# Optimization experiments

Measured on AMD Instinct MI355X. Metric: run time of the kernel, lower is better.

The kernel has to match this reference:

```python
import jax, jax.numpy as jnp
import numpy as np

K_TOP = 16
TEMP = 1.0
EPS = 1e-9

def setup_inputs() -> dict:
    key = jax.random.key(0)
    k1, k2, k3 = jax.random.split(key, 3)
    B, H, N, D = 4, 8, 2048, 64
    q = jax.random.normal(k1, (B, H, N, D), dtype=jnp.float32)
    k = jax.random.normal(k2, (B, H, N, D), dtype=jnp.float32)
    u = jax.random.uniform(k3, (B, N, N), dtype=jnp.float32)
    return {"q": q, "k": k, "u": u}

def reference(q, k, u):
    # q, k: [B, H, N, D]; u: uniform noise [B, N, N]
    d_head = q.shape[-1]
    scale = 1.0 / jnp.sqrt(jnp.asarray(d_head, dtype=q.dtype))
    # [B, H, N, N] scores, then mean over heads -> [B, N, N]
    attn_scores = jnp.einsum('bhnd,bhmd->bhnm', q, k) * scale
    logits = attn_scores.mean(axis=1)
    gumbel = -jnp.log(-jnp.log(u + EPS) + EPS)
    probs = jax.nn.softmax((logits + gumbel) / TEMP, axis=-1)
    topk_vals = jax.lax.top_k(probs, K_TOP)[0]          # [B, N, K]
    thresh = topk_vals.min(axis=-1, keepdims=True)      # [B, N, 1]
    sparse_mask = (probs >= thresh).astype(probs.dtype)
    return sparse_mask[:, None, :, :]                   # [B, 1, N, N]
```

## Files before the change

### kernel.cpp

```cpp
#include <hip/hip_runtime.h>
#include <math.h>

#define BB 4
#define HH 8
#define NN 2048
#define DD 64
#define KTOP 16
#define CUT_MARGIN 1e-3f

typedef _Float16 half_t;
typedef __attribute__((ext_vector_type(8))) _Float16 half8;
typedef __attribute__((ext_vector_type(4))) float floatx4;

__global__ __launch_bounds__(256, 2) void gemm_conv(const float* __restrict__ q,
                                                    const float* __restrict__ kk,
                                                    float* __restrict__ L) {
    const int flat = blockIdx.x;
    const int swz  = (flat & 7) * 128 + (flat >> 3);
    const int j0 = (swz & 15) * 128;
    const int i0 = ((swz >> 4) & 15) * 128;
    const int b  = swz >> 8;

    const int tid  = threadIdx.x;
    const int wave = __builtin_amdgcn_readfirstlane(tid >> 6);
    const int lane = tid & 63;
    const int wr = wave >> 1, wc = wave & 1;
    const int lm = lane & 15, quad = lane >> 4;

    __shared__ __align__(16) half_t Ah[8192];
    __shared__ __align__(16) half_t Al[8192];
    __shared__ __align__(16) half_t Bh[8192];
    __shared__ __align__(16) half_t Bl[8192];

    const float* gA = q  + ((size_t)(b * HH) * NN + i0) * DD;
    const float* gB = kk + ((size_t)(b * HH) * NN + j0) * DD;

    floatx4 acc1[4][4], acc2[4][4];
#pragma unroll
    for (int tr = 0; tr < 4; ++tr)
#pragma unroll
        for (int tc = 0; tc < 4; ++tc) {
            acc1[tr][tc] = (floatx4)0.0f;
            acc2[tr][tc] = (floatx4)0.0f;
        }

    for (int hh = 0; hh < HH; ++hh) {
        const float* ga = gA + (size_t)hh * (NN * DD);
        const float* gb = gB + (size_t)hh * (NN * DD);

        __syncthreads();

        float4 v0[8], v1[8];
#pragma unroll
        for (int i = 0; i < 4; ++i) {
            const int p = i * 256 + tid;
            v0[i]     = *(const float4*)(ga + (size_t)p * 8);
            v1[i]     = *(const float4*)(ga + (size_t)p * 8 + 4);
            v0[4 + i] = *(const float4*)(gb + (size_t)p * 8);
            v1[4 + i] = *(const float4*)(gb + (size_t)p * 8 + 4);
        }
#pragma unroll
        for (int i = 0; i < 8; ++i) {
            const int p  = (i & 3) * 256 + tid;
            const int r  = p >> 3;
            const int u8 = p & 7;
            const int off = (u8 >> 2) * 4096 + (r >> 3) * 256 +
                            (u8 & 3) * 64 + (r & 7) * 8;
            half_t* dh = (i < 4) ? Ah : Bh;
            half_t* dl = (i < 4) ? Al : Bl;
            float a[8] = {v0[i].x, v0[i].y, v0[i].z, v0[i].w,
                          v1[i].x, v1[i].y, v1[i].z, v1[i].w};
            half8 h, l;
#pragma unroll
            for (int e = 0; e < 8; ++e) {
                half_t hv = (half_t)a[e];
                h[e] = hv;
                l[e] = (half_t)((a[e] - (float)hv) * 2048.0f);
            }
            *(half8*)&dh[off] = h;
            *(half8*)&dl[off] = l;
        }

        __syncthreads();

#pragma unroll
        for (int ks = 0; ks < 2; ++ks) {
            half8 fah[4], fal[4], fbh[4], fbl[4];
#pragma unroll
            for (int t = 0; t < 4; ++t) {
                const int am = wr * 64 + t * 16 + lm;
                const int bm = wc * 64 + t * 16 + lm;
                const int ai = ks * 4096 + ((am >> 3) << 8) + (quad << 6) + ((am & 7) << 3);
                const int bi = ks * 4096 + ((bm >> 3) << 8) + (quad << 6) + ((bm & 7) << 3);
                fah[t] = *(const half8*)&Ah[ai];
                fal[t] = *(const half8*)&Al[ai];
                fbh[t] = *(const half8*)&Bh[bi];
                fbl[t] = *(const half8*)&Bl[bi];
            }
            __builtin_amdgcn_s_setprio(1);
#pragma unroll
            for (int tr = 0; tr < 4; ++tr)
#pragma unroll
                for (int tc = 0; tc < 4; ++tc) {
                    acc1[tr][tc] = __builtin_amdgcn_mfma_f32_16x16x32_f16(
                        fah[tr], fbh[tc], acc1[tr][tc], 0, 0, 0);
                    acc2[tr][tc] = __builtin_amdgcn_mfma_f32_16x16x32_f16(
                        fah[tr], fbl[tc], acc2[tr][tc], 0, 0, 0);
                    acc2[tr][tc] = __builtin_amdgcn_mfma_f32_16x16x32_f16(
                        fal[tr], fbh[tc], acc2[tr][tc], 0, 0, 0);
                }
            __builtin_amdgcn_s_setprio(0);
        }
    }

    const float s1 = 0.015625f;
    const float s2 = 0.015625f / 2048.0f;
#pragma unroll
    for (int tr = 0; tr < 4; ++tr)
#pragma unroll
        for (int r = 0; r < 4; ++r) {
            const int grow = i0 + wr * 64 + tr * 16 + quad * 4 + r;
            float* Lp = L + ((size_t)b * NN + grow) * NN + j0 + wc * 64 + lm;
#pragma unroll
            for (int tc = 0; tc < 4; ++tc)
                Lp[tc * 16] = acc1[tr][tc][r] * s1 + acc2[tr][tc][r] * s2;
        }
}

__device__ __forceinline__ unsigned long long flip64(double x) {
    unsigned long long v = (unsigned long long)__double_as_longlong(x);
    return v ^ ((0ULL - (v >> 63)) | 0x8000000000000000ULL);
}
__device__ __forceinline__ double unflip64(unsigned long long k) {
    unsigned long long v = (k >> 63) ? (k ^ 0x8000000000000000ULL) : ~k;
    return __longlong_as_double((long long)v);
}

__global__ __launch_bounds__(256) void topk_mask(float* __restrict__ LM,
                                                 const float* __restrict__ u) {
    const int wave = threadIdx.x >> 6;
    const int lane = threadIdx.x & 63;
    const int row  = blockIdx.x * 4 + wave;
    float* lrow = LM + (size_t)row * NN;
    const float* urow = u + (size_t)row * NN;

    __shared__ int s_idx[4][64];

    float z[32];
    unsigned hard = 0;
    float4 lb = *(const float4*)(lrow + lane * 4);
    float4 ub = *(const float4*)(urow + lane * 4);
#pragma unroll
    for (int e = 0; e < 8; ++e) {
        float4 lnx, unx;
        if (e < 7) {
            lnx = *(const float4*)(lrow + (e + 1) * 256 + lane * 4);
            unx = *(const float4*)(urow + (e + 1) * 256 + lane * 4);
        }
        const float* ls = (const float*)&lb;
        const float* us = (const float*)&ub;
#pragma unroll
        for (int s = 0; s < 4; ++s) {
            float w = -__logf(us[s] + 1e-9f);
            z[e * 4 + s] = ls[s] - __logf(w + 1e-9f);
            hard |= (us[s] > 0.999f ? 1u : 0u) << (e * 4 + s);
        }
        lb = lnx; ub = unx;
    }

    float v = z[0];
#pragma unroll
    for (int r = 1; r < 32; ++r) v = fmaxf(v, z[r]);
#pragma unroll
    for (int kS = 2; kS <= 64; kS <<= 1) {
#pragma unroll
        for (int j = kS >> 1; j > 0; j >>= 1) {
            float o = __shfl_xor(v, j, 64);
            bool asc = ((lane & kS) == 0);
            bool lower = ((lane & j) == 0);
            float mn = fminf(v, o), mx = fmaxf(v, o);
            v = (asc == lower) ? mn : mx;
        }
    }
    const float cut = __shfl(v, 48, 64) - CUT_MARGIN;

    int c = 0;
#pragma unroll
    for (int r = 0; r < 32; ++r) {
        bool p = (z[r] >= cut);
        unsigned long long m = __ballot(p);
        if (p) {
            int slot = c + __popcll(m & ((1ULL << lane) - 1ULL));
            if (slot < 64) s_idx[wave][slot] = (r >> 2) * 256 + lane * 4 + (r & 3);
        }
        c += __popcll(m);
    }
    if (c > 64) c = 64;

    unsigned long long key = 0xFFFFFFFFFFFFFFFFULL;
    if (lane < c) {
        int idx = s_idx[wave][lane];
        double uu = (double)urow[idx] + 1e-9;
        double w  = -log(uu);
        double g  = -log(w + 1e-9);
        key = flip64((double)lrow[idx] + g);
    }
#pragma unroll
    for (int kS = 2; kS <= 64; kS <<= 1) {
#pragma unroll
        for (int j = kS >> 1; j > 0; j >>= 1) {
            unsigned long long o = __shfl_xor(key, j, 64);
            bool asc = ((lane & kS) == 0);
            bool lower = ((lane & j) == 0);
            unsigned long long mn = (key < o) ? key : o;
            unsigned long long mx = (key < o) ? o : key;
            key = (asc == lower) ? mn : mx;
        }
    }
    const double thresh = unflip64(__shfl(key, c - KTOP, 64));

    const float t_hi = (float)thresh + 3e-4f;
    const float t_lo = (float)thresh - 3e-4f;
    unsigned bm = hard;
#pragma unroll
    for (int r = 0; r < 32; ++r)
        bm |= ((z[r] <= t_hi && z[r] >= t_lo) ? 1u : 0u) << r;
    while (bm) {
        int t = __builtin_ctz(bm);
        bm &= bm - 1;
        const int idx = (t >> 2) * 256 + lane * 4 + (t & 3);
        double uu = (double)urow[idx] + 1e-9;
        double w  = -log(uu);
        double g  = -log(w + 1e-9);
        double z64 = (double)lrow[idx] + g;
        z[t] = (z64 >= thresh) ? 1.0e30f : -1.0e30f;
    }

#pragma unroll
    for (int e = 0; e < 8; ++e) {
        float o[4];
#pragma unroll
        for (int s = 0; s < 4; ++s)
            o[s] = (z[e * 4 + s] > t_hi) ? 1.0f : 0.0f;
        *(float4*)(lrow + e * 256 + lane * 4) = *(float4*)o;
    }
}

extern "C" void kernel_launch(void* const* d_in, const int* in_sizes, int n_in,
                              void* d_out, int out_size, void* d_ws, size_t ws_size,
                              hipStream_t stream) {
    const float* q = (const float*)d_in[0];
    const float* k = (const float*)d_in[1];
    const float* u = (const float*)d_in[2];
    float* out = (float*)d_out;
    (void)d_ws; (void)ws_size;

    gemm_conv<<<(NN / 128) * (NN / 128) * BB, 256, 0, stream>>>(q, k, out);

    topk_mask<<<BB * NN / 4, 256, 0, stream>>>(out, u);
}
```

Baseline: 244.4 us.

## Prefetch next head's Q/K tiles into registers during MFMA compute

Global loads for the next head are now issued right after the LDS store barrier, so they overlap with the MFMA work on the current head instead of stalling at the top of each iteration. The lane-to-element mapping is also changed so each thread's LDS writes land at a precomputed offset, which aims to cut bank conflicts and index arithmetic. This keeps 16 float4 registers live across the MFMA loop, which raises register pressure and may affect occupancy at launch bounds of 2.

```diff
diff --git a/kernel.cpp b/kernel.cpp
--- a/kernel.cpp
+++ b/kernel.cpp
@@ -35,6 +35,11 @@
     const float* gA = q  + ((size_t)(b * HH) * NN + i0) * DD;
     const float* gB = kk + ((size_t)(b * HH) * NN + j0) * DD;
 
+    const int sa = lane >> 3;
+    const int sc = lane & 7;
+    const int plocal  = wave * 64 + sc * 8 + sa;
+    const int offbase = (sa >> 2) * 4096 + (sa & 3) * 64 + sc * 8 + wave * 256;
+
     floatx4 acc1[4][4], acc2[4][4];
 #pragma unroll
     for (int tr = 0; tr < 4; ++tr)
@@ -44,44 +49,48 @@
             acc2[tr][tc] = (floatx4)0.0f;
         }
 
+    float4 v0[8], v1[8];
+
+#define LOADREGS(hh_)                                                         \
+    {                                                                         \
+        const float* ga_ = gA + (size_t)(hh_) * (NN * DD);                    \
+        const float* gb_ = gB + (size_t)(hh_) * (NN * DD);                    \
+        _Pragma("unroll") for (int ib = 0; ib < 4; ++ib) {                    \
+            const int p = ib * 256 + plocal;                                  \
+            v0[ib]     = *(const float4*)(ga_ + (size_t)p * 8);               \
+            v1[ib]     = *(const float4*)(ga_ + (size_t)p * 8 + 4);           \
+            v0[4 + ib] = *(const float4*)(gb_ + (size_t)p * 8);               \
+            v1[4 + ib] = *(const float4*)(gb_ + (size_t)p * 8 + 4);           \
+        }                                                                     \
+    }
+
+    LOADREGS(0);
+
     for (int hh = 0; hh < HH; ++hh) {
-        const float* ga = gA + (size_t)hh * (NN * DD);
-        const float* gb = gB + (size_t)hh * (NN * DD);
-
         __syncthreads();
 
-        float4 v0[8], v1[8];
-#pragma unroll
-        for (int i = 0; i < 4; ++i) {
-            const int p = i * 256 + tid;
-            v0[i]     = *(const float4*)(ga + (size_t)p * 8);
-            v1[i]     = *(const float4*)(ga + (size_t)p * 8 + 4);
-            v0[4 + i] = *(const float4*)(gb + (size_t)p * 8);
-            v1[4 + i] = *(const float4*)(gb + (size_t)p * 8 + 4);
-        }
-#pragma unroll
-        for (int i = 0; i < 8; ++i) {
-            const int p  = (i & 3) * 256 + tid;
-            const int r  = p >> 3;
-            const int u8 = p & 7;
-            const int off = (u8 >> 2) * 4096 + (r >> 3) * 256 +
-                            (u8 & 3) * 64 + (r & 7) * 8;
-            half_t* dh = (i < 4) ? Ah : Bh;
-            half_t* dl = (i < 4) ? Al : Bl;
-            float a[8] = {v0[i].x, v0[i].y, v0[i].z, v0[i].w,
-                          v1[i].x, v1[i].y, v1[i].z, v1[i].w};
+#pragma unroll
+        for (int ii = 0; ii < 8; ++ii) {
+            const int ib = ii & 3;
+            half_t* dh = (ii < 4) ? Ah : Bh;
+            half_t* dl = (ii < 4) ? Al : Bl;
+            const int off = offbase + ib * 1024;
+            float aa[8] = {v0[ii].x, v0[ii].y, v0[ii].z, v0[ii].w,
+                           v1[ii].x, v1[ii].y, v1[ii].z, v1[ii].w};
             half8 h, l;
 #pragma unroll
             for (int e = 0; e < 8; ++e) {
-                half_t hv = (half_t)a[e];
+                half_t hv = (half_t)aa[e];
                 h[e] = hv;
-                l[e] = (half_t)((a[e] - (float)hv) * 2048.0f);
+                l[e] = (half_t)((aa[e] - (float)hv) * 2048.0f);
             }
             *(half8*)&dh[off] = h;
             *(half8*)&dl[off] = l;
         }
 
         __syncthreads();
+
+        if (hh < HH - 1) LOADREGS(hh + 1);
 
 #pragma unroll
         for (int ks = 0; ks < 2; ++ks) {
@@ -112,6 +121,7 @@
             __builtin_amdgcn_s_setprio(0);
         }
     }
+#undef LOADREGS
 
     const float s1 = 0.015625f;
     const float s2 = 0.015625f / 2048.0f;
```

New measurement: 284.6 us. 1.16x slower.
